# Kernel optimization log

Measured on AMD Instinct MI355X. Metric: run time of the kernel, lower is better.

Reference implementation:

```python
import jax, jax.numpy as jnp
import numpy as np


def setup_inputs() -> dict:
    key = jax.random.key(0)
    ks = jax.random.split(key, 6)
    B, Tq, Tv, H, A = 32, 1, 4096, 1024, 512
    return {
        "query": jax.random.normal(ks[0], (B, Tq, H), dtype=jnp.float32),
        "value": jax.random.normal(ks[1], (B, Tv, H), dtype=jnp.float32),
        # weights stored [in, out] (transpose of torch Linear's [out, in])
        "W_Q": jax.random.normal(ks[2], (H, A), dtype=jnp.float32) * 0.02,
        "W_V": jax.random.normal(ks[3], (H, A), dtype=jnp.float32) * 0.02,
        "bias": jax.random.uniform(ks[4], (A,), minval=-0.1, maxval=0.1, dtype=jnp.float32),
        "fc_w": jax.random.normal(ks[5], (A, 1), dtype=jnp.float32) * 0.02,
    }


def reference(query, value, W_Q, W_V, bias, fc_w):
    # query: [B, 1, H], value: [B, Tv, H]
    q_proj = jnp.einsum("bqh,ha->bqa", query, W_Q)          # [B, 1, A]
    v_proj = jnp.einsum("bth,ha->bta", value, W_V)          # [B, Tv, A]
    energy = jnp.tanh(q_proj + v_proj + bias)               # [B, Tv, A] (broadcast over Tv)
    attn_score = jnp.einsum("bta,ao->bt", energy, fc_w)     # [B, Tv]
    align = jax.nn.softmax(attn_score, axis=-1)             # [B, Tv]
    context = jnp.einsum("bt,bth->bh", align, value)        # [B, H]
    return context
```

## Files before the change

### kernel.cpp

```cpp
#include <hip/hip_runtime.h>
#include <hip/hip_bf16.h>
#include <math.h>

#define HH 1024
#define AA 512
#define TV 4096
#define NB 32

typedef __bf16 v8bf __attribute__((ext_vector_type(8)));
typedef float v4f __attribute__((ext_vector_type(4)));

__device__ __forceinline__ float fast_tanh(float x) {
  float e = __expf(2.0f * x);
  return 1.0f - 2.0f / (e + 1.0f);
}

__global__ void k_wt(const float* __restrict__ wv, __bf16* __restrict__ wt) {
  int idx = blockIdx.x * 256 + threadIdx.x;
  int k = idx >> 9;
  int n = idx & 511;
  wt[(size_t)n * HH + k] = (__bf16)wv[idx];
}

__global__ void k_qb(const float* __restrict__ query, const float* __restrict__ wq,
                     const float* __restrict__ bias, float* __restrict__ qb) {
  int b = blockIdx.x, hc = blockIdx.y;
  int a = threadIdx.x;
  __shared__ float ql[256];
  if (a < 256) ql[a] = query[b * HH + hc * 256 + a];
  __syncthreads();
  float s = (hc == 0) ? bias[a] : 0.0f;
  const float* w = wq + (size_t)(hc * 256) * AA + a;
  #pragma unroll 8
  for (int h = 0; h < 256; ++h) s += ql[h] * w[(size_t)h * AA];
  atomicAdd(&qb[b * AA + a], s);
}

#define BM 128
#define BK 32
#define LDA 40

__launch_bounds__(512, 1)
__global__ void k_score(const float* __restrict__ value, const __bf16* __restrict__ wt,
                        const float* __restrict__ qb, const float* __restrict__ fc,
                        float* __restrict__ scores) {
  __shared__ __align__(16) __bf16 As[BM * LDA];
  __shared__ __align__(16) __bf16 Bs[AA * LDA];
  __shared__ float s_red[BM * 4];

  const int tid  = threadIdx.x;
  const int lane = tid & 63, wave = tid >> 6;
  const int quad = lane >> 4, l15 = lane & 15;
  const int wm = wave & 1, wn = wave >> 1;

  const size_t m0 = (size_t)blockIdx.x * BM;
  const float* Ag = value + m0 * HH;

  const int am = tid >> 2, aq = tid & 3;

  v4f acc[4][8];
  #pragma unroll
  for (int i = 0; i < 4; ++i)
    #pragma unroll
    for (int n = 0; n < 8; ++n) { acc[i][n][0]=0.f; acc[i][n][1]=0.f; acc[i][n][2]=0.f; acc[i][n][3]=0.f; }

  for (int kk = 0; kk < HH; kk += BK) {
    const float* ap = Ag + (size_t)am * HH + kk + aq * 8;
    float4 f0 = *(const float4*)ap;
    float4 f1 = *(const float4*)(ap + 4);
    v8bf av;
    av[0]=(__bf16)f0.x; av[1]=(__bf16)f0.y; av[2]=(__bf16)f0.z; av[3]=(__bf16)f0.w;
    av[4]=(__bf16)f1.x; av[5]=(__bf16)f1.y; av[6]=(__bf16)f1.z; av[7]=(__bf16)f1.w;
    *(v8bf*)&As[am * LDA + aq * 8] = av;
    #pragma unroll
    for (int j = 0; j < 4; ++j) {
      int c = j * 512 + tid;
      int n = c >> 2, off = c & 3;
      uint4 d = *(const uint4*)(wt + (size_t)n * HH + kk + off * 8);
      *(uint4*)&Bs[n * LDA + off * 8] = d;
    }
    __syncthreads();
    v8bf af[4], bfr[8];
    #pragma unroll
    for (int i = 0; i < 4; ++i)
      af[i] = *(v8bf*)&As[(wm * 64 + i * 16 + l15) * LDA + quad * 8];
    #pragma unroll
    for (int n = 0; n < 8; ++n)
      bfr[n] = *(v8bf*)&Bs[(wn * 128 + n * 16 + l15) * LDA + quad * 8];
    #pragma unroll
    for (int i = 0; i < 4; ++i)
      #pragma unroll
      for (int n = 0; n < 8; ++n)
        acc[i][n] = __builtin_amdgcn_mfma_f32_16x16x32_bf16(af[i], bfr[n], acc[i][n], 0, 0, 0);
    __syncthreads();
  }

  const int bb = blockIdx.x >> 5;
  const int t0 = (blockIdx.x & 31) * BM;
  float fcl[8], qbl[8];
  #pragma unroll
  for (int n = 0; n < 8; ++n) {
    int col = wn * 128 + n * 16 + l15;
    fcl[n] = fc[col];
    qbl[n] = qb[bb * AA + col];
  }
  #pragma unroll
  for (int i = 0; i < 4; ++i) {
    #pragma unroll
    for (int j = 0; j < 4; ++j) {
      float p = 0.0f;
      #pragma unroll
      for (int n = 0; n < 8; ++n)
        p += fcl[n] * fast_tanh(acc[i][n][j] + qbl[n]);
      p += __shfl_xor(p, 1);
      p += __shfl_xor(p, 2);
      p += __shfl_xor(p, 4);
      p += __shfl_xor(p, 8);
      if (l15 == 0) {
        int row = wm * 64 + i * 16 + quad * 4 + j;
        s_red[row * 4 + wn] = p;
      }
    }
  }
  __syncthreads();
  if (tid < BM) {
    float s = s_red[tid * 4 + 0] + s_red[tid * 4 + 1] + s_red[tid * 4 + 2] + s_red[tid * 4 + 3];
    scores[(size_t)bb * TV + t0 + tid] = s;
  }
}

__global__ void k_softmax(float* __restrict__ scores) {
  int b = blockIdx.x;
  int tid = threadIdx.x;
  float* s = scores + (size_t)b * TV;
  float local[16];
  float mx = -1e30f;
  #pragma unroll
  for (int i = 0; i < 16; ++i) { local[i] = s[i * 256 + tid]; mx = fmaxf(mx, local[i]); }
  __shared__ float red[8];
  #pragma unroll
  for (int o = 32; o > 0; o >>= 1) mx = fmaxf(mx, __shfl_xor(mx, o));
  int wv = tid >> 6;
  if ((tid & 63) == 0) red[wv] = mx;
  __syncthreads();
  mx = fmaxf(fmaxf(red[0], red[1]), fmaxf(red[2], red[3]));
  float sum = 0.0f;
  #pragma unroll
  for (int i = 0; i < 16; ++i) { local[i] = __expf(local[i] - mx); sum += local[i]; }
  #pragma unroll
  for (int o = 32; o > 0; o >>= 1) sum += __shfl_xor(sum, o);
  if ((tid & 63) == 0) red[4 + wv] = sum;
  __syncthreads();
  float inv = 1.0f / (red[4] + red[5] + red[6] + red[7]);
  #pragma unroll
  for (int i = 0; i < 16; ++i) s[i * 256 + tid] = local[i] * inv;
}

__global__ void k_ctx_partial(const float* __restrict__ value, const float* __restrict__ align,
                              float* __restrict__ partial, int TC, int NC) {
  int tc = blockIdx.x, b = blockIdx.y;
  int tid = threadIdx.x;
  extern __shared__ float al[];
  for (int i = tid; i < TC; i += 256) al[i] = align[(size_t)b * TV + (size_t)tc * TC + i];
  __syncthreads();
  const float* vp = value + ((size_t)b * TV + (size_t)tc * TC) * HH + tid * 4;
  float ax = 0.f, ay = 0.f, az = 0.f, aw = 0.f;
  for (int t = 0; t < TC; ++t) {
    float4 v = *(const float4*)(vp + (size_t)t * HH);
    float a = al[t];
    ax = fmaf(a, v.x, ax); ay = fmaf(a, v.y, ay);
    az = fmaf(a, v.z, az); aw = fmaf(a, v.w, aw);
  }
  float4 o; o.x = ax; o.y = ay; o.z = az; o.w = aw;
  *(float4*)&partial[((size_t)(b * NC + tc)) * HH + tid * 4] = o;
}

__global__ void k_ctx_reduce(const float* __restrict__ partial, float* __restrict__ out, int NC) {
  int g = blockIdx.x * 256 + threadIdx.x;
  int b = g >> 10, h = g & 1023;
  float s = 0.0f;
  for (int c = 0; c < NC; ++c) s += partial[((size_t)(b * NC + c)) * HH + h];
  out[g] = s;
}

extern "C" void kernel_launch(void* const* d_in, const int* in_sizes, int n_in,
                              void* d_out, int out_size, void* d_ws, size_t ws_size,
                              hipStream_t stream) {
  const float* query = (const float*)d_in[0];
  const float* value = (const float*)d_in[1];
  const float* wq    = (const float*)d_in[2];
  const float* wv    = (const float*)d_in[3];
  const float* bias  = (const float*)d_in[4];
  const float* fc    = (const float*)d_in[5];
  float* out = (float*)d_out;

  char* ws = (char*)d_ws;
  __bf16* wt    = (__bf16*)ws;
  float*  qb    = (float*)(ws + (1 << 20));
  float*  scores= (float*)(ws + (1 << 20) + (1 << 16));
  size_t  base  = (1 << 20) + (1 << 16) + (1 << 19);
  float*  partial = (float*)(ws + base);

  int NC = 32;
  while (NC > 1 && base + (size_t)NB * NC * HH * 4 > ws_size) NC >>= 1;
  int TC = TV / NC;

  hipMemsetAsync(qb, 0, NB * AA * sizeof(float), stream);
  k_wt<<<2048, 256, 0, stream>>>(wv, wt);
  k_qb<<<dim3(NB, 4), 512, 0, stream>>>(query, wq, bias, qb);
  k_score<<<(NB * TV) / BM, 512, 0, stream>>>(value, wt, qb, fc, scores);
  k_softmax<<<NB, 256, 0, stream>>>(scores);
  k_ctx_partial<<<dim3(NC, NB), 256, TC * sizeof(float), stream>>>(value, scores, partial, TC, NC);
  k_ctx_reduce<<<(NB * HH) / 256, 256, 0, stream>>>(partial, out, NC);
}
```

Baseline: 1.017 ms.

## Load weight tiles via direct global-to-LDS with swizzled layout, prefetch A, smaller tiles

Pre-swizzles the transposed bf16 W_V so the score GEMM can copy B tiles straight into LDS with global_load_lds, dropping the register round-trip and LDS padding. Cuts the block to 64 rows with 4 waves and two blocks per CU, and prefetches the next value tile into registers during MFMA work. Also doubles the context split count and unrolls the context accumulation loop. The trade-off is that each block now re-reads the whole weight matrix for half as many rows, roughly doubling total weight traffic.

```diff
diff --git a/kernel.cpp b/kernel.cpp
--- a/kernel.cpp
+++ b/kernel.cpp
@@ -15,11 +15,23 @@
   return 1.0f - 2.0f / (e + 1.0f);
 }
 
-__global__ void k_wt(const float* __restrict__ wv, __bf16* __restrict__ wt) {
+__device__ __forceinline__ void load_lds16(const void* g, void* l) {
+  __builtin_amdgcn_global_load_lds(
+      (const __attribute__((address_space(1))) void*)g,
+      (__attribute__((address_space(3))) void*)l, 16, 0, 0);
+}
+
+__global__ void k_wt(const float* __restrict__ wv, __bf16* __restrict__ wt2) {
   int idx = blockIdx.x * 256 + threadIdx.x;
-  int k = idx >> 9;
-  int n = idx & 511;
-  wt[(size_t)n * HH + k] = (__bf16)wv[idx];
+  int n = idx >> 7;
+  int cl = idx & 127;
+  int g = cl >> 2, c = cl & 3;
+  int sw = (n >> 1) & 3;
+  int ks = g * 32 + ((c ^ sw) & 3) * 8;
+  v8bf o;
+  #pragma unroll
+  for (int j = 0; j < 8; ++j) o[j] = (__bf16)wv[(size_t)(ks + j) * AA + n];
+  *(v8bf*)&wt2[(size_t)n * HH + g * 32 + c * 8] = o;
 }
 
 __global__ void k_qb(const float* __restrict__ query, const float* __restrict__ wq,
@@ -36,27 +48,29 @@
   atomicAdd(&qb[b * AA + a], s);
 }
 
-#define BM 128
+#define BM 64
 #define BK 32
 #define LDA 40
 
-__launch_bounds__(512, 1)
-__global__ void k_score(const float* __restrict__ value, const __bf16* __restrict__ wt,
+__launch_bounds__(256, 2)
+__global__ void k_score(const float* __restrict__ value, const __bf16* __restrict__ wt2,
                         const float* __restrict__ qb, const float* __restrict__ fc,
                         float* __restrict__ scores) {
   __shared__ __align__(16) __bf16 As[BM * LDA];
-  __shared__ __align__(16) __bf16 Bs[AA * LDA];
+  __shared__ __align__(16) __bf16 Bs[AA * BK];
   __shared__ float s_red[BM * 4];
 
   const int tid  = threadIdx.x;
-  const int lane = tid & 63, wave = tid >> 6;
+  const int lane = tid & 63, w = tid >> 6;
   const int quad = lane >> 4, l15 = lane & 15;
-  const int wm = wave & 1, wn = wave >> 1;
+  const int swl  = (l15 >> 1) & 3;
+  const int bcol = ((quad ^ swl) & 3) * 8;
 
   const size_t m0 = (size_t)blockIdx.x * BM;
   const float* Ag = value + m0 * HH;
 
-  const int am = tid >> 2, aq = tid & 3;
+  const int ar = tid >> 2, ac = (tid & 3) * 8;
+  const int brow_l = lane >> 2, bchunk = (lane & 3) * 8;
 
   v4f acc[4][8];
   #pragma unroll
@@ -64,62 +78,67 @@
     #pragma unroll
     for (int n = 0; n < 8; ++n) { acc[i][n][0]=0.f; acc[i][n][1]=0.f; acc[i][n][2]=0.f; acc[i][n][3]=0.f; }
 
+  const float* ap0 = Ag + (size_t)ar * HH + ac;
+  float4 a0 = *(const float4*)ap0;
+  float4 a1 = *(const float4*)(ap0 + 4);
+
   for (int kk = 0; kk < HH; kk += BK) {
-    const float* ap = Ag + (size_t)am * HH + kk + aq * 8;
-    float4 f0 = *(const float4*)ap;
-    float4 f1 = *(const float4*)(ap + 4);
-    v8bf av;
-    av[0]=(__bf16)f0.x; av[1]=(__bf16)f0.y; av[2]=(__bf16)f0.z; av[3]=(__bf16)f0.w;
-    av[4]=(__bf16)f1.x; av[5]=(__bf16)f1.y; av[6]=(__bf16)f1.z; av[7]=(__bf16)f1.w;
-    *(v8bf*)&As[am * LDA + aq * 8] = av;
-    #pragma unroll
-    for (int j = 0; j < 4; ++j) {
-      int c = j * 512 + tid;
-      int n = c >> 2, off = c & 3;
-      uint4 d = *(const uint4*)(wt + (size_t)n * HH + kk + off * 8);
-      *(uint4*)&Bs[n * LDA + off * 8] = d;
-    }
     __syncthreads();
+    #pragma unroll
+    for (int i = 0; i < 8; ++i) {
+      int r0 = w * 128 + i * 16;
+      load_lds16(wt2 + (size_t)(r0 + brow_l) * HH + kk + bchunk, (void*)&Bs[r0 * BK]);
+    }
+    {
+      v8bf av;
+      av[0]=(__bf16)a0.x; av[1]=(__bf16)a0.y; av[2]=(__bf16)a0.z; av[3]=(__bf16)a0.w;
+      av[4]=(__bf16)a1.x; av[5]=(__bf16)a1.y; av[6]=(__bf16)a1.z; av[7]=(__bf16)a1.w;
+      *(v8bf*)&As[ar * LDA + ac] = av;
+    }
+    __syncthreads();
+    if (kk + BK < HH) {
+      const float* apn = Ag + (size_t)ar * HH + kk + BK + ac;
+      a0 = *(const float4*)apn;
+      a1 = *(const float4*)(apn + 4);
+    }
     v8bf af[4], bfr[8];
     #pragma unroll
-    for (int i = 0; i < 4; ++i)
-      af[i] = *(v8bf*)&As[(wm * 64 + i * 16 + l15) * LDA + quad * 8];
-    #pragma unroll
-    for (int n = 0; n < 8; ++n)
-      bfr[n] = *(v8bf*)&Bs[(wn * 128 + n * 16 + l15) * LDA + quad * 8];
-    #pragma unroll
-    for (int i = 0; i < 4; ++i)
+    for (int mt = 0; mt < 4; ++mt)
+      af[mt] = *(v8bf*)&As[(mt * 16 + l15) * LDA + quad * 8];
+    #pragma unroll
+    for (int nt = 0; nt < 8; ++nt) {
+      int n = w * 128 + nt * 16 + l15;
+      bfr[nt] = *(v8bf*)&Bs[n * BK + bcol];
+    }
+    #pragma unroll
+    for (int mt = 0; mt < 4; ++mt)
       #pragma unroll
-      for (int n = 0; n < 8; ++n)
-        acc[i][n] = __builtin_amdgcn_mfma_f32_16x16x32_bf16(af[i], bfr[n], acc[i][n], 0, 0, 0);
-    __syncthreads();
-  }
-
-  const int bb = blockIdx.x >> 5;
-  const int t0 = (blockIdx.x & 31) * BM;
+      for (int nt = 0; nt < 8; ++nt)
+        acc[mt][nt] = __builtin_amdgcn_mfma_f32_16x16x32_bf16(af[mt], bfr[nt], acc[mt][nt], 0, 0, 0);
+  }
+
+  const int bb = blockIdx.x >> 6;
+  const int t0 = (blockIdx.x & 63) * BM;
   float fcl[8], qbl[8];
   #pragma unroll
-  for (int n = 0; n < 8; ++n) {
-    int col = wn * 128 + n * 16 + l15;
-    fcl[n] = fc[col];
-    qbl[n] = qb[bb * AA + col];
-  }
-  #pragma unroll
-  for (int i = 0; i < 4; ++i) {
+  for (int nt = 0; nt < 8; ++nt) {
+    int col = w * 128 + nt * 16 + l15;
+    fcl[nt] = fc[col];
+    qbl[nt] = qb[bb * AA + col];
+  }
+  #pragma unroll
+  for (int mt = 0; mt < 4; ++mt) {
     #pragma unroll
     for (int j = 0; j < 4; ++j) {
       float p = 0.0f;
       #pragma unroll
-      for (int n = 0; n < 8; ++n)
-        p += fcl[n] * fast_tanh(acc[i][n][j] + qbl[n]);
+      for (int nt = 0; nt < 8; ++nt)
+        p += fcl[nt] * fast_tanh(acc[mt][nt][j] + qbl[nt]);
       p += __shfl_xor(p, 1);
       p += __shfl_xor(p, 2);
       p += __shfl_xor(p, 4);
       p += __shfl_xor(p, 8);
-      if (l15 == 0) {
-        int row = wm * 64 + i * 16 + quad * 4 + j;
-        s_red[row * 4 + wn] = p;
-      }
+      if (l15 == 0) s_red[(mt * 16 + quad * 4 + j) * 4 + w] = p;
     }
   }
   __syncthreads();
@@ -165,6 +184,7 @@
   __syncthreads();
   const float* vp = value + ((size_t)b * TV + (size_t)tc * TC) * HH + tid * 4;
   float ax = 0.f, ay = 0.f, az = 0.f, aw = 0.f;
+  #pragma unroll 8
   for (int t = 0; t < TC; ++t) {
     float4 v = *(const float4*)(vp + (size_t)t * HH);
     float a = al[t];
@@ -195,20 +215,20 @@
   float* out = (float*)d_out;
 
   char* ws = (char*)d_ws;
-  __bf16* wt    = (__bf16*)ws;
+  __bf16* wt2   = (__bf16*)ws;
   float*  qb    = (float*)(ws + (1 << 20));
   float*  scores= (float*)(ws + (1 << 20) + (1 << 16));
   size_t  base  = (1 << 20) + (1 << 16) + (1 << 19);
   float*  partial = (float*)(ws + base);
 
-  int NC = 32;
+  int NC = 64;
   while (NC > 1 && base + (size_t)NB * NC * HH * 4 > ws_size) NC >>= 1;
   int TC = TV / NC;
 
   hipMemsetAsync(qb, 0, NB * AA * sizeof(float), stream);
-  k_wt<<<2048, 256, 0, stream>>>(wv, wt);
+  k_wt<<<256, 256, 0, stream>>>(wv, wt2);
   k_qb<<<dim3(NB, 4), 512, 0, stream>>>(query, wq, bias, qb);
-  k_score<<<(NB * TV) / BM, 512, 0, stream>>>(value, wt, qb, fc, scores);
+  k_score<<<(NB * TV) / BM, 256, 0, stream>>>(value, wt2, qb, fc, scores);
   k_softmax<<<NB, 256, 0, stream>>>(scores);
   k_ctx_partial<<<dim3(NC, NB), 256, TC * sizeof(float), stream>>>(value, scores, partial, TC, NC);
   k_ctx_reduce<<<(NB * HH) / 256, 256, 0, stream>>>(partial, out, NC);
```

Result: faster. 942.5 us (-7.4%).
